# Kernel tuning notes

Measured on AMD Instinct MI355X. Metric: run time of the kernel, lower is better.

## Reference

```python
import jax, jax.numpy as jnp
import numpy as np

D = 512       # d_model
H = 8         # n_heads
L = 6         # n_blocks
DFF = 2048    # d_ffn
IN_DIM = 4096
OUT_DIM = 1000
B = 8
S = 512
DK = D // H
EPS = 1e-5
NEG = -1e9    # masked_fill value from source (-1000000000.0)

# sinusoidal positional encoding table (matches Positional_Encoding)
_pos = np.arange(5000)[:, None].astype(np.float64)
_div = np.exp(np.arange(0, D, 2) * (-np.log(10000.0) / D))
_pe = np.zeros((5000, D), np.float32)
_pe[:, 0::2] = np.sin(_pos * _div)
_pe[:, 1::2] = np.cos(_pos * _div)
PE = jnp.asarray(_pe)


def _ln(x, g, b):
    m = jnp.mean(x, -1, keepdims=True)
    v = jnp.var(x, -1, keepdims=True)
    return (x - m) * jax.lax.rsqrt(v + EPS) * g + b


def _attn(q, k, v, causal):
    # q:[B,Sq,D], k/v:[B,Sk,D] -> multi-head attention with source's quirky mask
    b, sq, _ = q.shape
    sk = k.shape[1]
    q = q.reshape(b, sq, H, DK).transpose(0, 2, 1, 3)
    k = k.reshape(b, sk, H, DK).transpose(0, 2, 1, 3)
    v = v.reshape(b, sk, H, DK).transpose(0, 2, 1, 3)
    s = jnp.einsum('bhqd,bhkd->bhqk', q, k) / jnp.sqrt(jnp.asarray(DK, q.dtype))
    mask = s != 0.0  # faithful: source masks positions where score == padding (0)
    if causal:
        mask = mask & jnp.tril(jnp.ones((sq, sk), bool))
    s = jnp.where(mask, s, NEG)
    p = jax.nn.softmax(s, axis=-1)
    o = jnp.einsum('bhqk,bhkd->bhqd', p, v)
    return o.transpose(0, 2, 1, 3).reshape(b, sq, D)


def _ffn(x, w1, b1, w2, b2):
    return jax.nn.relu(x @ w1 + b1) @ w2 + b2


def setup_inputs() -> dict:
    key = jax.random.key(0)
    ks = iter(jax.random.split(key, 40))

    def w(shape, s=0.02):
        return jax.random.normal(next(ks), shape, jnp.float32) * s

    inp = {}
    inp['x'] = jax.random.randint(next(ks), (B, S), 0, IN_DIM)
    inp['target'] = jax.random.randint(next(ks), (B,), 0, OUT_DIM)
    inp['in_emb'] = w((IN_DIM, D), 1.0)
    inp['out_emb'] = w((OUT_DIM, D), 1.0)
    # encoder params (stacked over layers)
    inp['enc_qkv_w'] = w((L, 3, D, D))
    inp['enc_qkv_b'] = w((L, 3, D))
    inp['enc_ln1_g'] = jnp.ones((L, D), jnp.float32)
    inp['enc_ln1_b'] = jnp.zeros((L, D), jnp.float32)
    inp['enc_ffn1_w'] = w((L, D, DFF))
    inp['enc_ffn1_b'] = w((L, DFF))
    inp['enc_ffn2_w'] = w((L, DFF, D))
    inp['enc_ffn2_b'] = w((L, D))
    inp['enc_ln2_g'] = jnp.ones((L, D), jnp.float32)
    inp['enc_ln2_b'] = jnp.zeros((L, D), jnp.float32)
    # decoder params
    inp['dec_qkv1_w'] = w((L, 3, D, D))
    inp['dec_qkv1_b'] = w((L, 3, D))
    inp['dec_ln1_g'] = jnp.ones((L, D), jnp.float32)
    inp['dec_ln1_b'] = jnp.zeros((L, D), jnp.float32)
    inp['dec_qkv2_w'] = w((L, 3, D, D))
    inp['dec_qkv2_b'] = w((L, 3, D))
    inp['dec_ln2_g'] = jnp.ones((L, D), jnp.float32)
    inp['dec_ln2_b'] = jnp.zeros((L, D), jnp.float32)
    inp['dec_ffn1_w'] = w((L, D, DFF))
    inp['dec_ffn1_b'] = w((L, DFF))
    inp['dec_ffn2_w'] = w((L, DFF, D))
    inp['dec_ffn2_b'] = w((L, D))
    inp['dec_ln3_g'] = jnp.ones((L, D), jnp.float32)
    inp['dec_ln3_b'] = jnp.zeros((L, D), jnp.float32)
    inp['out_w'] = w((D, OUT_DIM))
    inp['out_b'] = w((OUT_DIM,))
    return inp


def reference(x, target, in_emb, out_emb,
              enc_qkv_w, enc_qkv_b, enc_ln1_g, enc_ln1_b,
              enc_ffn1_w, enc_ffn1_b, enc_ffn2_w, enc_ffn2_b,
              enc_ln2_g, enc_ln2_b,
              dec_qkv1_w, dec_qkv1_b, dec_ln1_g, dec_ln1_b,
              dec_qkv2_w, dec_qkv2_b, dec_ln2_g, dec_ln2_b,
              dec_ffn1_w, dec_ffn1_b, dec_ffn2_w, dec_ffn2_b,
              dec_ln3_g, dec_ln3_b, out_w, out_b):
    scale = jnp.sqrt(jnp.float32(D))
    # encoder: embed tokens + positional encoding (dropout is identity at eval)
    e = in_emb[x] * scale + PE[None, :S]
    for i in range(L):
        q = e @ enc_qkv_w[i, 0] + enc_qkv_b[i, 0]
        k = e @ enc_qkv_w[i, 1] + enc_qkv_b[i, 1]
        v = e @ enc_qkv_w[i, 2] + enc_qkv_b[i, 2]
        e = _ln(_attn(q, k, v, False) + e, enc_ln1_g[i], enc_ln1_b[i])
        e = _ln(e + _ffn(e, enc_ffn1_w[i], enc_ffn1_b[i], enc_ffn2_w[i], enc_ffn2_b[i]),
                enc_ln2_g[i], enc_ln2_b[i])
    # decoder: target.unsqueeze(1) -> seq len 1
    d = out_emb[target][:, None, :] * scale + PE[None, :1]
    for i in range(L):
        q = d @ dec_qkv1_w[i, 0] + dec_qkv1_b[i, 0]
        k = d @ dec_qkv1_w[i, 1] + dec_qkv1_b[i, 1]
        v = d @ dec_qkv1_w[i, 2] + dec_qkv1_b[i, 2]
        d = _ln(_attn(q, k, v, True) + d, dec_ln1_g[i], dec_ln1_b[i])
        q = d @ dec_qkv2_w[i, 0] + dec_qkv2_b[i, 0]
        k = e @ dec_qkv2_w[i, 1] + dec_qkv2_b[i, 1]
        v = e @ dec_qkv2_w[i, 2] + dec_qkv2_b[i, 2]
        d = _ln(_attn(q, k, v, False) + d, dec_ln2_g[i], dec_ln2_b[i])
        d = _ln(d + _ffn(d, dec_ffn1_w[i], dec_ffn1_b[i], dec_ffn2_w[i], dec_ffn2_b[i]),
                dec_ln3_g[i], dec_ln3_b[i])
    return d @ out_w + out_b  # [B, 1, OUT_DIM] logits (source never applies its softmax)
```

## Files before the change

### kernel.cpp

```cpp
#include <hip/hip_runtime.h>
#include <hip/hip_bf16.h>

#define DM 512
#define NH 8
#define DK 64
#define SEQ 512
#define NB 8
#define NL 6
#define DFF 2048
#define OUTD 1000
#define EMB_SCALE 22.627416997969522f
#define PE_C (-0.017988946039015984)

typedef __bf16 bf16x8 __attribute__((ext_vector_type(8)));
typedef __bf16 bf16x4 __attribute__((ext_vector_type(4)));
typedef float f32x4 __attribute__((ext_vector_type(4)));

__device__ __forceinline__ void load16_lds(const __bf16* g, __bf16* l) {
  __builtin_amdgcn_global_load_lds(
      (const __attribute__((address_space(1))) void*)g,
      (__attribute__((address_space(3))) void*)l, 16, 0, 0);
}

__device__ __forceinline__ float dot8(bf16x8 w, const float* a) {
  float s = 0.f;
#pragma unroll
  for (int j = 0; j < 8; ++j) s += (float)w[j] * a[j];
  return s;
}

__global__ __launch_bounds__(256) void pe_kernel(float* __restrict__ pe) {
  int s = blockIdx.x;
  int d2 = threadIdx.x;
  double div = exp((double)(2 * d2) * PE_C);
  double arg = (double)s * div;
  pe[(size_t)s * DM + 2 * d2] = (float)sin(arg);
  pe[(size_t)s * DM + 2 * d2 + 1] = (float)cos(arg);
}

__global__ __launch_bounds__(256) void embed_enc(const int* __restrict__ x,
                                                 const float* __restrict__ emb,
                                                 const float* __restrict__ pe,
                                                 float* __restrict__ e,
                                                 __bf16* __restrict__ eb) {
  int idx = blockIdx.x * 256 + threadIdx.x;
  int d = idx & (DM - 1);
  int bs = idx >> 9;
  int s = bs & (SEQ - 1);
  int tok = x[bs];
  float v = emb[(size_t)tok * DM + d] * EMB_SCALE + pe[(size_t)s * DM + d];
  e[idx] = v;
  eb[idx] = (__bf16)v;
}

__global__ __launch_bounds__(256) void embed_dec(const int* __restrict__ t,
                                                 const float* __restrict__ emb,
                                                 float* __restrict__ dd) {
  int idx = blockIdx.x * 256 + threadIdx.x;
  int d = idx & (DM - 1);
  int b = idx >> 9;
  float pe = (d & 1) ? 1.0f : 0.0f;
  dd[idx] = emb[(size_t)t[b] * DM + d] * EMB_SCALE + pe;
}

__global__ __launch_bounds__(256) void transpose_w(const float* __restrict__ W,
                                                   __bf16* __restrict__ WT,
                                                   int K, int N) {
  __shared__ float t[32][33];
  size_t off = (size_t)blockIdx.z * K * N;
  W += off; WT += off;
  int k0 = blockIdx.y * 32, n0 = blockIdx.x * 32;
  int tx = threadIdx.x & 7, ty = threadIdx.x >> 3;
  float4 v = *(const float4*)&W[(size_t)(k0 + ty) * N + n0 + tx * 4];
  t[ty][tx * 4 + 0] = v.x; t[ty][tx * 4 + 1] = v.y;
  t[ty][tx * 4 + 2] = v.z; t[ty][tx * 4 + 3] = v.w;
  __syncthreads();
  bf16x4 o;
  o[0] = (__bf16)t[tx * 4 + 0][ty];
  o[1] = (__bf16)t[tx * 4 + 1][ty];
  o[2] = (__bf16)t[tx * 4 + 2][ty];
  o[3] = (__bf16)t[tx * 4 + 3][ty];
  *(bf16x4*)&WT[(size_t)(n0 + ty) * K + k0 + tx * 4] = o;
}

__global__ __launch_bounds__(256) void transpose_ow(const float* __restrict__ W,
                                                    __bf16* __restrict__ WT) {
  __shared__ float t[32][33];
  int n0 = blockIdx.x * 32, k0 = blockIdx.y * 32;
  int tid = threadIdx.x;
  for (int i = tid; i < 1024; i += 256) {
    int kk = i >> 5, nn = i & 31;
    t[kk][nn] = (n0 + nn < OUTD) ? W[(size_t)(k0 + kk) * OUTD + n0 + nn] : 0.f;
  }
  __syncthreads();
  for (int i = tid; i < 1024; i += 256) {
    int nn = i >> 5, kk = i & 31;
    if (n0 + nn < OUTD)
      WT[(size_t)(n0 + nn) * DM + k0 + kk] = (__bf16)t[kk][nn];
  }
}

template <int BN, bool RELU, bool WF32, bool WBF16, bool TRV, bool KVM>
__global__ __launch_bounds__(256) void mfma_gemm(
    const __bf16* __restrict__ A, const __bf16* __restrict__ BT,
    const float* __restrict__ bias, float* __restrict__ C,
    __bf16* __restrict__ Cb, __bf16* __restrict__ Vt, int M, int N, int K,
    long btStride, long bStride, long cStride) {
  int z = blockIdx.z;
  if (KVM) {
    long idx = (long)(z >> 1) * 3 + 1 + (z & 1);
    BT += idx * btStride;
    bias += idx * bStride;
  } else {
    BT += (size_t)z * btStride;
    bias += (size_t)z * bStride;
  }
  if (WF32) C += (size_t)z * cStride;
  if (WBF16) Cb += (size_t)z * cStride;

  constexpr int NI = BN / 32;
  __shared__ __bf16 As[128 * 64];
  __shared__ __bf16 Bs[BN * 64];

  int tid = threadIdx.x;
  int wave = tid >> 6, lane = tid & 63;
  int wm = wave >> 1, wn = wave & 1;
  int quad = lane >> 4, l16 = lane & 15;
  int rlane = lane >> 3, c8 = lane & 7;
  int m0 = blockIdx.y * 128, n0 = blockIdx.x * BN;
  int gcol = ((c8 ^ rlane) * 8);

  f32x4 acc[4][NI];
#pragma unroll
  for (int i = 0; i < 4; ++i)
#pragma unroll
    for (int j = 0; j < NI; ++j) acc[i][j] = (f32x4){0.f, 0.f, 0.f, 0.f};

  for (int k0 = 0; k0 < K; k0 += 64) {
    __syncthreads();
#pragma unroll
    for (int j = 0; j < 4; ++j) {
      int row = j * 32 + wave * 8 + rlane;
      load16_lds(&A[(size_t)(m0 + row) * K + k0 + gcol],
                 &As[(j * 32 + wave * 8) * 64]);
    }
#pragma unroll
    for (int j = 0; j < BN / 32; ++j) {
      int row = j * 32 + wave * 8 + rlane;
      load16_lds(&BT[(size_t)(n0 + row) * K + k0 + gcol],
                 &Bs[(j * 32 + wave * 8) * 64]);
    }
    __syncthreads();
#pragma unroll
    for (int kk = 0; kk < 64; kk += 32) {
      bf16x8 af[4], bf[NI];
#pragma unroll
      for (int i = 0; i < 4; ++i) {
        int row = wm * 64 + i * 16 + l16;
        af[i] = *(const bf16x8*)&As[row * 64 + ((((kk >> 3) + quad) ^ (row & 7)) * 8)];
      }
#pragma unroll
      for (int i = 0; i < NI; ++i) {
        int row = wn * (BN / 2) + i * 16 + l16;
        bf[i] = *(const bf16x8*)&Bs[row * 64 + ((((kk >> 3) + quad) ^ (row & 7)) * 8)];
      }
#pragma unroll
      for (int mi = 0; mi < 4; ++mi)
#pragma unroll
        for (int ni = 0; ni < NI; ++ni)
          acc[mi][ni] = __builtin_amdgcn_mfma_f32_16x16x32_bf16(
              af[mi], bf[ni], acc[mi][ni], 0, 0, 0);
    }
  }

#pragma unroll
  for (int ni = 0; ni < NI; ++ni) {
    int col = n0 + wn * (BN / 2) + ni * 16 + l16;
    float bv = bias[col];
    if (TRV && z == 2) {
      int b = m0 >> 9;
#pragma unroll
      for (int mi = 0; mi < 4; ++mi) {
        int srow = (m0 & 511) + wm * 64 + mi * 16 + quad * 4;
        bf16x4 pk;
#pragma unroll
        for (int r = 0; r < 4; ++r) pk[r] = (__bf16)(acc[mi][ni][r] + bv);
        *(bf16x4*)&Vt[((size_t)(b * 512 + col)) * 512 + srow] = pk;
      }
    } else {
#pragma unroll
      for (int mi = 0; mi < 4; ++mi) {
#pragma unroll
        for (int r = 0; r < 4; ++r) {
          int row = m0 + wm * 64 + mi * 16 + quad * 4 + r;
          float v = acc[mi][ni][r] + bv;
          if (RELU) v = fmaxf(v, 0.f);
          if (WF32) C[(size_t)row * N + col] = v;
          if (WBF16) Cb[(size_t)row * N + col] = (__bf16)v;
        }
      }
    }
  }
}

#define SCP 520
__global__ __launch_bounds__(256) void attn_mfma(const __bf16* __restrict__ QKV,
                                                 const __bf16* __restrict__ Vt,
                                                 float* __restrict__ O) {
  __shared__ __bf16 Sc[16 * SCP];
  __shared__ __bf16 Tt[64 * 64];

  const long ACTL = (long)NB * SEQ * DM;
  int tid = threadIdx.x;
  int wave = tid >> 6, lane = tid & 63;
  int quad = lane >> 4, l16 = lane & 15;
  int rlane = lane >> 3, c8 = lane & 7;
  int q0 = blockIdx.x * 16;
  int bh = blockIdx.y, b = bh >> 3, h = bh & 7;
  const __bf16* Q = QKV;
  const __bf16* Kp = QKV + ACTL;
  size_t baseQ = ((size_t)b * SEQ + q0) * DM + h * DK;
  size_t baseK = ((size_t)b * SEQ) * DM + h * DK;
  const __bf16* VtB = Vt + ((size_t)(b * 512 + h * 64)) * 512;
  int gcol = (c8 ^ rlane) * 8;

  bf16x8 af0 = *(const bf16x8*)&Q[baseQ + (size_t)l16 * DM + quad * 8];
  bf16x8 af1 = *(const bf16x8*)&Q[baseQ + (size_t)l16 * DM + 32 + quad * 8];

  for (int kt = 0; kt < 8; ++kt) {
    __syncthreads();
#pragma unroll
    for (int j = 0; j < 2; ++j) {
      int row = j * 32 + wave * 8 + rlane;
      load16_lds(&Kp[baseK + (size_t)(kt * 64 + row) * DM + gcol],
                 &Tt[(j * 32 + wave * 8) * 64]);
    }
    __syncthreads();
    f32x4 acc = (f32x4){0.f, 0.f, 0.f, 0.f};
    int krow = wave * 16 + l16, sw = krow & 7;
    bf16x8 b0 = *(const bf16x8*)&Tt[krow * 64 + ((quad ^ sw) * 8)];
    bf16x8 b1 = *(const bf16x8*)&Tt[krow * 64 + (((4 + quad) ^ sw) * 8)];
    acc = __builtin_amdgcn_mfma_f32_16x16x32_bf16(af0, b0, acc, 0, 0, 0);
    acc = __builtin_amdgcn_mfma_f32_16x16x32_bf16(af1, b1, acc, 0, 0, 0);
#pragma unroll
    for (int r = 0; r < 4; ++r)
      Sc[(quad * 4 + r) * SCP + kt * 64 + wave * 16 + l16] =
          (__bf16)(acc[r] * 0.125f);
  }
  __syncthreads();

#pragma unroll
  for (int rr = 0; rr < 4; ++rr) {
    int r = wave * 4 + rr;
    float v[8];
    float mx = -1e30f;
#pragma unroll
    for (int j = 0; j < 8; ++j) {
      v[j] = (float)Sc[r * SCP + j * 64 + lane];
      mx = fmaxf(mx, v[j]);
    }
    for (int o = 32; o > 0; o >>= 1) mx = fmaxf(mx, __shfl_xor(mx, o));
    float sum = 0.f;
#pragma unroll
    for (int j = 0; j < 8; ++j) { v[j] = __expf(v[j] - mx); sum += v[j]; }
    for (int o = 32; o > 0; o >>= 1) sum += __shfl_xor(sum, o);
    float inv = 1.f / sum;
#pragma unroll
    for (int j = 0; j < 8; ++j)
      Sc[r * SCP + j * 64 + lane] = (__bf16)(v[j] * inv);
  }

  f32x4 oacc = (f32x4){0.f, 0.f, 0.f, 0.f};
  for (int kt = 0; kt < 8; ++kt) {
    __syncthreads();
#pragma unroll
    for (int j = 0; j < 2; ++j) {
      int row = j * 32 + wave * 8 + rlane;
      load16_lds(&VtB[(size_t)row * 512 + kt * 64 + gcol],
                 &Tt[(j * 32 + wave * 8) * 64]);
    }
    __syncthreads();
    int drow = wave * 16 + l16, sw = drow & 7;
#pragma unroll
    for (int kk = 0; kk < 64; kk += 32) {
      bf16x8 pa = *(const bf16x8*)&Sc[l16 * SCP + kt * 64 + kk + quad * 8];
      bf16x8 vb = *(const bf16x8*)&Tt[drow * 64 + ((((kk >> 3) + quad) ^ sw) * 8)];
      oacc = __builtin_amdgcn_mfma_f32_16x16x32_bf16(pa, vb, oacc, 0, 0, 0);
    }
  }
#pragma unroll
  for (int r = 0; r < 4; ++r)
    O[((size_t)b * SEQ + q0 + quad * 4 + r) * DM + h * DK + wave * 16 + l16] =
        oacc[r];
}

template <bool WB>
__global__ __launch_bounds__(256) void add_ln(
    const float* __restrict__ x, const float* __restrict__ res,
    const float* __restrict__ cbias,
    const float* __restrict__ g, const float* __restrict__ beta,
    float* __restrict__ y, __bf16* __restrict__ yb) {
  int row = blockIdx.x;
  int tid = threadIdx.x;
  const float* xr = x + (size_t)row * DM;
  const float* rr = res + (size_t)row * DM;
  float b0 = cbias ? cbias[tid] : 0.f;
  float b1 = cbias ? cbias[tid + 256] : 0.f;
  float v0 = xr[tid] + b0 + rr[tid];
  float v1 = xr[tid + 256] + b1 + rr[tid + 256];
  float s = v0 + v1, sq = v0 * v0 + v1 * v1;
  for (int o = 32; o > 0; o >>= 1) {
    s += __shfl_xor(s, o);
    sq += __shfl_xor(sq, o);
  }
  __shared__ float ps[4], pq[4];
  int wv = tid >> 6;
  if ((tid & 63) == 0) { ps[wv] = s; pq[wv] = sq; }
  __syncthreads();
  s = ps[0] + ps[1] + ps[2] + ps[3];
  sq = pq[0] + pq[1] + pq[2] + pq[3];
  float mean = s * (1.f / DM);
  float var = sq * (1.f / DM) - mean * mean;
  float rstd = rsqrtf(var + 1e-5f);
  float o0 = (v0 - mean) * rstd * g[tid] + beta[tid];
  float o1 = (v1 - mean) * rstd * g[tid + 256] + beta[tid + 256];
  y[(size_t)row * DM + tid] = o0;
  y[(size_t)row * DM + tid + 256] = o1;
  if (WB) {
    yb[(size_t)row * DM + tid] = (__bf16)o0;
    yb[(size_t)row * DM + tid + 256] = (__bf16)o1;
  }
}


__global__ __launch_bounds__(256) void dec_vln(
    float* __restrict__ dd, const __bf16* __restrict__ WvT,
    const float* __restrict__ bv, const float* __restrict__ g,
    const float* __restrict__ beta) {
  __shared__ float arow[DM];
  int r = blockIdx.x, tid = threadIdx.x;
  arow[tid] = dd[(size_t)r * DM + tid];
  arow[tid + 256] = dd[(size_t)r * DM + tid + 256];
  __syncthreads();
  float out[2];
#pragma unroll
  for (int cc = 0; cc < 2; ++cc) {
    int c = tid + cc * 256;
    const __bf16* w = &WvT[(size_t)c * DM];
    float acc = 0.f;
#pragma unroll 4
    for (int k = 0; k < DM; k += 8) acc += dot8(*(const bf16x8*)&w[k], &arow[k]);
    out[cc] = arow[c] + acc + bv[c];
  }
  float s = out[0] + out[1], sq = out[0] * out[0] + out[1] * out[1];
  for (int o = 32; o > 0; o >>= 1) { s += __shfl_xor(s, o); sq += __shfl_xor(sq, o); }
  __shared__ float ps[4], pq[4];
  int wv = tid >> 6;
  if ((tid & 63) == 0) { ps[wv] = s; pq[wv] = sq; }
  __syncthreads();
  s = ps[0] + ps[1] + ps[2] + ps[3];
  sq = pq[0] + pq[1] + pq[2] + pq[3];
  float mean = s * (1.f / DM);
  float rstd = rsqrtf(sq * (1.f / DM) - mean * mean + 1e-5f);
  dd[(size_t)r * DM + tid] = (out[0] - mean) * rstd * g[tid] + beta[tid];
  dd[(size_t)r * DM + tid + 256] = (out[1] - mean) * rstd * g[tid + 256] + beta[tid + 256];
}

__global__ __launch_bounds__(256) void dec_qattn(
    const float* __restrict__ dd, const __bf16* __restrict__ WqT,
    const float* __restrict__ qb, const __bf16* __restrict__ Kb,
    const __bf16* __restrict__ Vb, float* __restrict__ da) {
  __shared__ float arow[DM];
  __shared__ float red[4][64];
  __shared__ float q[64];
  __shared__ float sc[SEQ];
  __shared__ float wred[4];
  __shared__ float smax, ssum;

  int bh = blockIdx.x, b = bh >> 3, h = bh & 7;
  int tid = threadIdx.x, lane = tid & 63, wave = tid >> 6;
  arow[tid] = dd[(size_t)b * DM + tid];
  arow[tid + 256] = dd[(size_t)b * DM + tid + 256];
  __syncthreads();

  {
    int c = tid & 63, s = tid >> 6;
    const __bf16* w = &WqT[(size_t)(h * 64 + c) * DM + s * 128];
    float acc = 0.f;
#pragma unroll
    for (int k = 0; k < 128; k += 8) acc += dot8(*(const bf16x8*)&w[k], &arow[s * 128 + k]);
    red[s][c] = acc;
  }
  __syncthreads();
  if (tid < 64) q[tid] = red[0][tid] + red[1][tid] + red[2][tid] + red[3][tid] + qb[h * 64 + tid];
  __syncthreads();

  for (int key = tid; key < SEQ; key += 256) {
    const __bf16* kp = &Kb[((size_t)b * SEQ + key) * DM + h * 64];
    float acc = 0.f;
#pragma unroll
    for (int k = 0; k < 64; k += 8) acc += dot8(*(const bf16x8*)&kp[k], &q[k]);
    sc[key] = acc * 0.125f;
  }
  __syncthreads();
  float m = -1e30f;
  for (int j = tid; j < SEQ; j += 256) m = fmaxf(m, sc[j]);
  for (int o = 32; o > 0; o >>= 1) m = fmaxf(m, __shfl_xor(m, o));
  if (lane == 0) wred[wave] = m;
  __syncthreads();
  m = fmaxf(fmaxf(wred[0], wred[1]), fmaxf(wred[2], wred[3]));
  float sum = 0.f;
  for (int j = tid; j < SEQ; j += 256) {
    float p = __expf(sc[j] - m);
    sc[j] = p;
    sum += p;
  }
  for (int o = 32; o > 0; o >>= 1) sum += __shfl_xor(sum, o);
  __syncthreads();
  if (lane == 0) wred[wave] = sum;
  __syncthreads();
  float inv = 1.f / (wred[0] + wred[1] + wred[2] + wred[3]);

  {
    int d = tid & 63, s = tid >> 6;
    float acc = 0.f;
    const __bf16* vp = &Vb[((size_t)b * SEQ + s * 128) * DM + h * 64 + d];
#pragma unroll 8
    for (int k = 0; k < 128; ++k) acc += sc[s * 128 + k] * (float)vp[(size_t)k * DM];
    red[s][d] = acc;
  }
  __syncthreads();
  if (tid < 64)
    da[(size_t)b * DM + h * 64 + tid] =
        (red[0][tid] + red[1][tid] + red[2][tid] + red[3][tid]) * inv;
}

__global__ __launch_bounds__(256) void dec_ffn1(
    const float* __restrict__ dd, const __bf16* __restrict__ W1T,
    const float* __restrict__ b1, float* __restrict__ h) {
  __shared__ float a[8][DM];
  int tid = threadIdx.x, lane = tid & 63, wave = tid >> 6;
  for (int i = tid; i < 8 * DM; i += 256) a[i >> 9][i & 511] = dd[i];
  __syncthreads();
  int col = blockIdx.x * 4 + wave;
  bf16x8 w = *(const bf16x8*)&W1T[(size_t)col * DM + lane * 8];
  float acc[8];
#pragma unroll
  for (int r = 0; r < 8; ++r) acc[r] = dot8(w, &a[r][lane * 8]);
#pragma unroll
  for (int r = 0; r < 8; ++r)
    for (int o = 32; o > 0; o >>= 1) acc[r] += __shfl_xor(acc[r], o);
  if (lane == 0) {
    float bb = b1[col];
#pragma unroll
    for (int r = 0; r < 8; ++r) h[(size_t)r * DFF + col] = fmaxf(acc[r] + bb, 0.f);
  }
}

__global__ __launch_bounds__(256) void dec_ffn2(
    const float* __restrict__ h, const __bf16* __restrict__ W2T,
    const float* __restrict__ b2, float* __restrict__ df) {
  __shared__ float red[4][8];
  int tid = threadIdx.x, lane = tid & 63, wave = tid >> 6;
  int c = wave >> 1, half = wave & 1;
  int col = blockIdx.x * 2 + c;
  int k0 = half * 1024 + lane * 8;
  bf16x8 w0 = *(const bf16x8*)&W2T[(size_t)col * DFF + k0];
  bf16x8 w1 = *(const bf16x8*)&W2T[(size_t)col * DFF + k0 + 512];
  float acc[8];
#pragma unroll
  for (int r = 0; r < 8; ++r) {
    float4 h0a = *(const float4*)&h[(size_t)r * DFF + k0];
    float4 h0b = *(const float4*)&h[(size_t)r * DFF + k0 + 4];
    float4 h1a = *(const float4*)&h[(size_t)r * DFF + k0 + 512];
    float4 h1b = *(const float4*)&h[(size_t)r * DFF + k0 + 516];
    float hh0[8] = {h0a.x, h0a.y, h0a.z, h0a.w, h0b.x, h0b.y, h0b.z, h0b.w};
    float hh1[8] = {h1a.x, h1a.y, h1a.z, h1a.w, h1b.x, h1b.y, h1b.z, h1b.w};
    acc[r] = dot8(w0, hh0) + dot8(w1, hh1);
  }
#pragma unroll
  for (int r = 0; r < 8; ++r)
    for (int o = 32; o > 0; o >>= 1) acc[r] += __shfl_xor(acc[r], o);
  if (lane == 0) {
#pragma unroll
    for (int r = 0; r < 8; ++r) red[wave][r] = acc[r];
  }
  __syncthreads();
  if (tid < 16) {
    int cc = tid >> 3, r = tid & 7;
    int ocol = blockIdx.x * 2 + cc;
    df[(size_t)r * DM + ocol] =
        red[cc * 2][r] + red[cc * 2 + 1][r] + b2[ocol];
  }
}

__global__ __launch_bounds__(256) void dec_out(
    const float* __restrict__ dd, const __bf16* __restrict__ WoT,
    const float* __restrict__ ob, float* __restrict__ out) {
  __shared__ float a[8][DM];
  int tid = threadIdx.x, lane = tid & 63, wave = tid >> 6;
  for (int i = tid; i < 8 * DM; i += 256) a[i >> 9][i & 511] = dd[i];
  __syncthreads();
  int col = blockIdx.x * 4 + wave;
  bf16x8 w = *(const bf16x8*)&WoT[(size_t)col * DM + lane * 8];
  float acc[8];
#pragma unroll
  for (int r = 0; r < 8; ++r) acc[r] = dot8(w, &a[r][lane * 8]);
#pragma unroll
  for (int r = 0; r < 8; ++r)
    for (int o = 32; o > 0; o >>= 1) acc[r] += __shfl_xor(acc[r], o);
  if (lane == 0) {
    float bb = ob[col];
#pragma unroll
    for (int r = 0; r < 8; ++r) out[(size_t)r * OUTD + col] = acc[r] + bb;
  }
}

extern "C" void kernel_launch(void* const* d_in, const int* in_sizes, int n_in,
                              void* d_out, int out_size, void* d_ws, size_t ws_size,
                              hipStream_t stream) {
  const int* x = (const int*)d_in[0];
  const int* target = (const int*)d_in[1];
  const float* in_emb = (const float*)d_in[2];
  const float* out_emb = (const float*)d_in[3];
  const float* enc_qkv_w = (const float*)d_in[4];
  const float* enc_qkv_b = (const float*)d_in[5];
  const float* enc_ln1_g = (const float*)d_in[6];
  const float* enc_ln1_b = (const float*)d_in[7];
  const float* enc_ffn1_w = (const float*)d_in[8];
  const float* enc_ffn1_b = (const float*)d_in[9];
  const float* enc_ffn2_w = (const float*)d_in[10];
  const float* enc_ffn2_b = (const float*)d_in[11];
  const float* enc_ln2_g = (const float*)d_in[12];
  const float* enc_ln2_b = (const float*)d_in[13];
  const float* dec_qkv1_w = (const float*)d_in[14];
  const float* dec_qkv1_b = (const float*)d_in[15];
  const float* dec_ln1_g = (const float*)d_in[16];
  const float* dec_ln1_b = (const float*)d_in[17];
  const float* dec_qkv2_w = (const float*)d_in[18];
  const float* dec_qkv2_b = (const float*)d_in[19];
  const float* dec_ln2_g = (const float*)d_in[20];
  const float* dec_ln2_b = (const float*)d_in[21];
  const float* dec_ffn1_w = (const float*)d_in[22];
  const float* dec_ffn1_b = (const float*)d_in[23];
  const float* dec_ffn2_w = (const float*)d_in[24];
  const float* dec_ffn2_b = (const float*)d_in[25];
  const float* dec_ln3_g = (const float*)d_in[26];
  const float* dec_ln3_b = (const float*)d_in[27];
  const float* out_w = (const float*)d_in[28];
  const float* out_b = (const float*)d_in[29];

  const long ACTL = (long)NB * SEQ * DM;
  const int M = NB * SEQ;
  const long WQS = (long)DM * DM;
  const long WFS = (long)DM * DFF;

  char* p = (char*)d_ws;
  float* e = (float*)p;            p += ACTL * 4;
  float* tb = (float*)p;           p += ACTL * 4;
  float* pe = (float*)p;           p += (long)SEQ * DM * 4;
  float* dd = (float*)p;           p += NB * DM * 4;
  float* da = (float*)p;           p += NB * DM * 4;
  float* dh = (float*)p;           p += NB * DFF * 4;
  float* df = (float*)p;           p += NB * DM * 4;
  p = (char*)(((uintptr_t)p + 255) & ~(uintptr_t)255);
  __bf16* eb = (__bf16*)p;         p += ACTL * 2;
  __bf16* qkvb = (__bf16*)p;       p += 3 * ACTL * 2;
  __bf16* hbb = (__bf16*)p;        p += (long)M * DFF * 2;
  __bf16* kvb = (__bf16*)p;        p += 12L * ACTL * 2;
  __bf16* wtq = (__bf16*)p;        p += 18L * WQS * 2;
  __bf16* wtf1 = (__bf16*)p;       p += 6L * WFS * 2;
  __bf16* wtf2 = (__bf16*)p;       p += 6L * WFS * 2;
  __bf16* wtd = (__bf16*)p;        p += 18L * WQS * 2;
  __bf16* wtd1 = (__bf16*)p;       p += 18L * WQS * 2;
  __bf16* wf1t = (__bf16*)p;       p += 6L * WFS * 2;
  __bf16* wf2t = (__bf16*)p;       p += 6L * WFS * 2;
  __bf16* wot = (__bf16*)p;        p += (long)OUTD * DM * 2;

  __bf16* vtb = qkvb + 2 * ACTL;

  pe_kernel<<<SEQ, 256, 0, stream>>>(pe);
  transpose_w<<<dim3(16, 16, 18), 256, 0, stream>>>(enc_qkv_w, wtq, DM, DM);
  transpose_w<<<dim3(64, 16, 6), 256, 0, stream>>>(enc_ffn1_w, wtf1, DM, DFF);
  transpose_w<<<dim3(16, 64, 6), 256, 0, stream>>>(enc_ffn2_w, wtf2, DFF, DM);
  transpose_w<<<dim3(16, 16, 18), 256, 0, stream>>>(dec_qkv2_w, wtd, DM, DM);
  transpose_w<<<dim3(16, 16, 18), 256, 0, stream>>>(dec_qkv1_w, wtd1, DM, DM);
  transpose_w<<<dim3(64, 16, 6), 256, 0, stream>>>(dec_ffn1_w, wf1t, DM, DFF);
  transpose_w<<<dim3(16, 64, 6), 256, 0, stream>>>(dec_ffn2_w, wf2t, DFF, DM);
  transpose_ow<<<dim3(32, 16), 256, 0, stream>>>(out_w, wot);

  embed_enc<<<(M * DM) / 256, 256, 0, stream>>>(x, in_emb, pe, e, eb);
  for (int i = 0; i < NL; ++i) {
    mfma_gemm<128, false, false, true, true, false><<<dim3(4, 32, 3), 256, 0, stream>>>(
        eb, wtq + (size_t)i * 3 * WQS, enc_qkv_b + (size_t)i * 3 * DM,
        nullptr, qkvb, vtb, M, DM, DM, WQS, DM, ACTL);
    attn_mfma<<<dim3(SEQ / 16, NB * NH), 256, 0, stream>>>(qkvb, vtb, tb);
    add_ln<true><<<M, 256, 0, stream>>>(tb, e, nullptr, enc_ln1_g + i * DM,
                                        enc_ln1_b + i * DM, e, eb);
    mfma_gemm<128, true, false, true, false, false><<<dim3(16, 32, 1), 256, 0, stream>>>(
        eb, wtf1 + (size_t)i * WFS, enc_ffn1_b + (size_t)i * DFF,
        nullptr, hbb, nullptr, M, DFF, DM, 0, 0, 0);
    mfma_gemm<64, false, true, false, false, false><<<dim3(8, 32, 1), 256, 0, stream>>>(
        hbb, wtf2 + (size_t)i * WFS, enc_ffn2_b + (size_t)i * DM,
        tb, nullptr, nullptr, M, DM, DFF, 0, 0, 0);
    add_ln<true><<<M, 256, 0, stream>>>(tb, e, nullptr, enc_ln2_g + i * DM,
                                        enc_ln2_b + i * DM, e, eb);
  }

  mfma_gemm<128, false, false, true, false, true><<<dim3(4, 32, 12), 256, 0, stream>>>(
      eb, wtd, dec_qkv2_b, nullptr, kvb, nullptr, M, DM, DM, WQS, DM, ACTL);

  embed_dec<<<(NB * DM) / 256, 256, 0, stream>>>(target, out_emb, dd);
  for (int i = 0; i < NL; ++i) {
    dec_vln<<<8, 256, 0, stream>>>(
        dd, wtd1 + ((size_t)i * 3 + 2) * WQS, dec_qkv1_b + ((size_t)i * 3 + 2) * DM,
        dec_ln1_g + i * DM, dec_ln1_b + i * DM);
    dec_qattn<<<64, 256, 0, stream>>>(
        dd, wtd + (size_t)i * 3 * WQS, dec_qkv2_b + (size_t)i * 3 * DM,
        kvb + (size_t)i * 2 * ACTL, kvb + ((size_t)i * 2 + 1) * ACTL, da);
    add_ln<false><<<NB, 256, 0, stream>>>(
        da, dd, nullptr, dec_ln2_g + i * DM, dec_ln2_b + i * DM, dd, nullptr);
    dec_ffn1<<<DFF / 4, 256, 0, stream>>>(
        dd, wf1t + (size_t)i * WFS, dec_ffn1_b + (size_t)i * DFF, dh);
    dec_ffn2<<<DM / 2, 256, 0, stream>>>(
        dh, wf2t + (size_t)i * WFS, dec_ffn2_b + (size_t)i * DM, df);
    add_ln<false><<<NB, 256, 0, stream>>>(
        df, dd, nullptr, dec_ln3_g + i * DM, dec_ln3_b + i * DM, dd, nullptr);
  }

  dec_out<<<OUTD / 4, 256, 0, stream>>>(dd, wot, out_b, (float*)d_out);
}
```

Before: 1.227 ms.

## Double-buffer LDS tiles in MFMA GEMM and attention kernels

Adds ping-pong LDS buffers to the GEMM K-loop and to the attention K and V loops. The next tile's global-to-LDS load is issued before the MFMAs on the current tile, and the two barriers per iteration become one. This is meant to hide global load latency behind matrix math, at the cost of doubled LDS use, which may lower occupancy. The positional-encoding kernel also moves from double to float transcendentals, which is cheaper but slightly less precise.

Result: no change. 1.225 ms (-0.2%).

```diff
diff --git a/kernel.cpp b/kernel.cpp
--- a/kernel.cpp
+++ b/kernel.cpp
@@ -10,7 +10,7 @@
 #define DFF 2048
 #define OUTD 1000
 #define EMB_SCALE 22.627416997969522f
-#define PE_C (-0.017988946039015984)
+#define PE_C (-0.017988946039015984f)
 
 typedef __bf16 bf16x8 __attribute__((ext_vector_type(8)));
 typedef __bf16 bf16x4 __attribute__((ext_vector_type(4)));
@@ -32,10 +32,10 @@
 __global__ __launch_bounds__(256) void pe_kernel(float* __restrict__ pe) {
   int s = blockIdx.x;
   int d2 = threadIdx.x;
-  double div = exp((double)(2 * d2) * PE_C);
-  double arg = (double)s * div;
-  pe[(size_t)s * DM + 2 * d2] = (float)sin(arg);
-  pe[(size_t)s * DM + 2 * d2 + 1] = (float)cos(arg);
+  float div = expf((float)(2 * d2) * PE_C);
+  float arg = (float)s * div;
+  pe[(size_t)s * DM + 2 * d2] = sinf(arg);
+  pe[(size_t)s * DM + 2 * d2 + 1] = cosf(arg);
 }
 
 __global__ __launch_bounds__(256) void embed_enc(const int* __restrict__ x,
@@ -119,8 +119,8 @@
   if (WBF16) Cb += (size_t)z * cStride;
 
   constexpr int NI = BN / 32;
-  __shared__ __bf16 As[128 * 64];
-  __shared__ __bf16 Bs[BN * 64];
+  __shared__ __bf16 As[2][128 * 64];
+  __shared__ __bf16 Bs[2][BN * 64];
 
   int tid = threadIdx.x;
   int wave = tid >> 6, lane = tid & 63;
@@ -136,33 +136,39 @@
 #pragma unroll
     for (int j = 0; j < NI; ++j) acc[i][j] = (f32x4){0.f, 0.f, 0.f, 0.f};
 
-  for (int k0 = 0; k0 < K; k0 += 64) {
-    __syncthreads();
+  auto stage = [&](int buf, int k0) {
 #pragma unroll
     for (int j = 0; j < 4; ++j) {
       int row = j * 32 + wave * 8 + rlane;
       load16_lds(&A[(size_t)(m0 + row) * K + k0 + gcol],
-                 &As[(j * 32 + wave * 8) * 64]);
+                 &As[buf][(j * 32 + wave * 8) * 64]);
     }
 #pragma unroll
     for (int j = 0; j < BN / 32; ++j) {
       int row = j * 32 + wave * 8 + rlane;
       load16_lds(&BT[(size_t)(n0 + row) * K + k0 + gcol],
-                 &Bs[(j * 32 + wave * 8) * 64]);
-    }
-    __syncthreads();
+                 &Bs[buf][(j * 32 + wave * 8) * 64]);
+    }
+  };
+
+  const int NT = K >> 6;
+  stage(0, 0);
+  __syncthreads();
+  for (int t = 0; t < NT; ++t) {
+    int cur = t & 1;
+    if (t + 1 < NT) stage(cur ^ 1, (t + 1) << 6);
 #pragma unroll
     for (int kk = 0; kk < 64; kk += 32) {
       bf16x8 af[4], bf[NI];
 #pragma unroll
       for (int i = 0; i < 4; ++i) {
         int row = wm * 64 + i * 16 + l16;
-        af[i] = *(const bf16x8*)&As[row * 64 + ((((kk >> 3) + quad) ^ (row & 7)) * 8)];
+        af[i] = *(const bf16x8*)&As[cur][row * 64 + ((((kk >> 3) + quad) ^ (row & 7)) * 8)];
       }
 #pragma unroll
       for (int i = 0; i < NI; ++i) {
         int row = wn * (BN / 2) + i * 16 + l16;
-        bf[i] = *(const bf16x8*)&Bs[row * 64 + ((((kk >> 3) + quad) ^ (row & 7)) * 8)];
+        bf[i] = *(const bf16x8*)&Bs[cur][row * 64 + ((((kk >> 3) + quad) ^ (row & 7)) * 8)];
       }
 #pragma unroll
       for (int mi = 0; mi < 4; ++mi)
@@ -171,6 +177,7 @@
           acc[mi][ni] = __builtin_amdgcn_mfma_f32_16x16x32_bf16(
               af[mi], bf[ni], acc[mi][ni], 0, 0, 0);
     }
+    __syncthreads();
   }
 
 #pragma unroll
@@ -208,7 +215,7 @@
                                                  const __bf16* __restrict__ Vt,
                                                  float* __restrict__ O) {
   __shared__ __bf16 Sc[16 * SCP];
-  __shared__ __bf16 Tt[64 * 64];
+  __shared__ __bf16 Tt[2][64 * 64];
 
   const long ACTL = (long)NB * SEQ * DM;
   int tid = threadIdx.x;
@@ -227,27 +234,42 @@
   bf16x8 af0 = *(const bf16x8*)&Q[baseQ + (size_t)l16 * DM + quad * 8];
   bf16x8 af1 = *(const bf16x8*)&Q[baseQ + (size_t)l16 * DM + 32 + quad * 8];
 
-  for (int kt = 0; kt < 8; ++kt) {
-    __syncthreads();
+  auto stageK = [&](int buf, int kt) {
 #pragma unroll
     for (int j = 0; j < 2; ++j) {
       int row = j * 32 + wave * 8 + rlane;
       load16_lds(&Kp[baseK + (size_t)(kt * 64 + row) * DM + gcol],
-                 &Tt[(j * 32 + wave * 8) * 64]);
-    }
-    __syncthreads();
+                 &Tt[buf][(j * 32 + wave * 8) * 64]);
+    }
+  };
+  auto stageV = [&](int buf, int kt) {
+#pragma unroll
+    for (int j = 0; j < 2; ++j) {
+      int row = j * 32 + wave * 8 + rlane;
+      load16_lds(&VtB[(size_t)row * 512 + kt * 64 + gcol],
+                 &Tt[buf][(j * 32 + wave * 8) * 64]);
+    }
+  };
+
+  stageK(0, 0);
+  __syncthreads();
+  for (int kt = 0; kt < 8; ++kt) {
+    int cur = kt & 1;
+    if (kt < 7) stageK(cur ^ 1, kt + 1);
     f32x4 acc = (f32x4){0.f, 0.f, 0.f, 0.f};
     int krow = wave * 16 + l16, sw = krow & 7;
-    bf16x8 b0 = *(const bf16x8*)&Tt[krow * 64 + ((quad ^ sw) * 8)];
-    bf16x8 b1 = *(const bf16x8*)&Tt[krow * 64 + (((4 + quad) ^ sw) * 8)];
+    bf16x8 b0 = *(const bf16x8*)&Tt[cur][krow * 64 + ((quad ^ sw) * 8)];
+    bf16x8 b1 = *(const bf16x8*)&Tt[cur][krow * 64 + (((4 + quad) ^ sw) * 8)];
     acc = __builtin_amdgcn_mfma_f32_16x16x32_bf16(af0, b0, acc, 0, 0, 0);
     acc = __builtin_amdgcn_mfma_f32_16x16x32_bf16(af1, b1, acc, 0, 0, 0);
 #pragma unroll
     for (int r = 0; r < 4; ++r)
       Sc[(quad * 4 + r) * SCP + kt * 64 + wave * 16 + l16] =
           (__bf16)(acc[r] * 0.125f);
-  }
-  __syncthreads();
+    __syncthreads();
+  }
+
+  stageV(0, 0);
 
 #pragma unroll
   for (int rr = 0; rr < 4; ++rr) {
@@ -269,24 +291,20 @@
     for (int j = 0; j < 8; ++j)
       Sc[r * SCP + j * 64 + lane] = (__bf16)(v[j] * inv);
   }
+  __syncthreads();
 
   f32x4 oacc = (f32x4){0.f, 0.f, 0.f, 0.f};
   for (int kt = 0; kt < 8; ++kt) {
-    __syncthreads();
-#pragma unroll
-    for (int j = 0; j < 2; ++j) {
-      int row = j * 32 + wave * 8 + rlane;
-      load16_lds(&VtB[(size_t)row * 512 + kt * 64 + gcol],
-                 &Tt[(j * 32 + wave * 8) * 64]);
-    }
-    __syncthreads();
+    int cur = kt & 1;
+    if (kt < 7) stageV(cur ^ 1, kt + 1);
     int drow = wave * 16 + l16, sw = drow & 7;
 #pragma unroll
     for (int kk = 0; kk < 64; kk += 32) {
       bf16x8 pa = *(const bf16x8*)&Sc[l16 * SCP + kt * 64 + kk + quad * 8];
-      bf16x8 vb = *(const bf16x8*)&Tt[drow * 64 + ((((kk >> 3) + quad) ^ sw) * 8)];
+      bf16x8 vb = *(const bf16x8*)&Tt[cur][drow * 64 + ((((kk >> 3) + quad) ^ sw) * 8)];
       oacc = __builtin_amdgcn_mfma_f32_16x16x32_bf16(pa, vb, oacc, 0, 0, 0);
     }
+    __syncthreads();
   }
 #pragma unroll
   for (int r = 0; r < 4; ++r)
@@ -375,7 +393,6 @@
   __shared__ float q[64];
   __shared__ float sc[SEQ];
   __shared__ float wred[4];
-  __shared__ float smax, ssum;
 
   int bh = blockIdx.x, b = bh >> 3, h = bh & 7;
   int tid = threadIdx.x, lane = tid & 63, wave = tid >> 6;
```
